# Kernel tuning notes

Measured on AMD Instinct MI355X. Metric: run time of the kernel, lower is better.

The kernel has to match this reference:

```python
import jax, jax.numpy as jnp
import numpy as np

N_FFT = 512
HOP = 256
HID = 512
VOCAB = 44
NB_BINS = 257  # n_fft//2 + 1, == max_bin
NEG = -100000.0
POS = 200000.0


def _hann(n):
    # torch.hann_window is periodic: 0.5*(1-cos(2*pi*k/N))
    return 0.5 * (1.0 - jnp.cos(2.0 * jnp.pi * jnp.arange(n, dtype=jnp.float32) / n))


def _stft_mag(x):
    # x: (B, C, T) -> (frames, B, C(mono=1), bins), magnitude spectrogram (power=1, mono mean)
    B, C, T = x.shape
    nfr = 1 + (T - N_FFT) // HOP
    idx = jnp.arange(nfr)[:, None] * HOP + jnp.arange(N_FFT)[None, :]
    frames = x.reshape(B * C, T)[:, idx] * _hann(N_FFT)      # (BC, F, n_fft)
    mag = jnp.abs(jnp.fft.rfft(frames, axis=-1))             # (BC, F, bins)
    mag = mag.reshape(B, C, nfr, N_FFT // 2 + 1).mean(axis=1, keepdims=True)
    return mag.transpose(2, 0, 1, 3)                          # (F, B, 1, bins)


def _lstm(x, wih, whh, b, reverse):
    # x: (T, B, in). torch gate order i, f, g, o. Returns hidden states (T, B, H).
    Bt, H = x.shape[1], whh.shape[1]
    def step(carry, xt):
        h, c = carry
        g = xt @ wih.T + h @ whh.T + b
        i, f, gg, o = jnp.split(g, 4, axis=-1)
        c = jax.nn.sigmoid(f) * c + jax.nn.sigmoid(i) * jnp.tanh(gg)
        h = jax.nn.sigmoid(o) * jnp.tanh(c)
        return (h, c), h
    init = (jnp.zeros((Bt, H), x.dtype), jnp.zeros((Bt, H), x.dtype))
    _, hs = jax.lax.scan(step, init, x, reverse=reverse)
    return hs


def _bilstm(x, wih, whh, b):
    # wih: (2, 4H, in) [fwd, bwd]
    hf = _lstm(x, wih[0], whh[0], b[0], False)
    hb = _lstm(x, wih[1], whh[1], b[1], True)
    return jnp.concatenate([hf, hb], axis=-1)


def _bn(x, g, b):
    # BatchNorm1d in training mode: batch statistics over axis 0, eps=1e-5
    mu = x.mean(0)
    v = ((x - mu) ** 2).mean(0)
    return g * (x - mu) * jax.lax.rsqrt(v + 1e-5) + b


def _dtw(scores):
    # dtw[n,m] = scores[n-1,m-1] + max(dtw[n-1,m], dtw[n-1,m-1]); row-wise scan
    B, N, M = scores.shape
    row0 = jnp.full((B, M + 1), NEG, scores.dtype).at[:, 0].set(POS)
    negcol = jnp.full((B, 1), NEG, scores.dtype)
    def step(prev, s):  # prev: (B, M+1), s: (B, M)
        shifted = jnp.concatenate([negcol, prev[:, :-1]], axis=1)
        new = jnp.concatenate([negcol, s + jnp.maximum(prev, shifted)[:, 1:]], axis=1)
        return new, new[:, 1:]
    _, rows = jax.lax.scan(step, row0, scores.transpose(1, 0, 2))  # (N, B, M)
    return rows.transpose(1, 0, 2)


def setup_inputs() -> dict:
    key = jax.random.key(0)
    ks = jax.random.split(key, 10)
    B, T, L = 8, 524544, 512
    s = 0.05
    H2 = HID // 2  # per-direction hidden = 256
    return {
        "x_audio": jax.random.normal(ks[0], (B, 1, T), jnp.float32),
        "text_idx": jax.random.randint(ks[1], (B, L), 0, VOCAB),
        "txt_wih": jax.random.normal(ks[2], (2, 4 * H2, VOCAB), jnp.float32) * s,
        "txt_whh": jax.random.normal(ks[3], (2, 4 * H2, H2), jnp.float32) * s,
        "txt_b": jax.random.normal(ks[4], (2, 4 * H2), jnp.float32) * s,
        "w_s": jax.random.normal(ks[5], (HID, HID), jnp.float32) / np.sqrt(HID).astype(np.float32),
        "fc1_w": jax.random.normal(ks[6], (HID, NB_BINS), jnp.float32) * s,
        "bn1_g": jnp.ones((HID,), jnp.float32),
        "bn1_b": jnp.zeros((HID,), jnp.float32),
        "input_mean": jnp.zeros((NB_BINS,), jnp.float32),
        "input_scale": jnp.ones((NB_BINS,), jnp.float32),
        "ae_wih": jax.random.normal(ks[7], (2, 2, 4 * H2, HID), jnp.float32) * s,
        "ae_whh": jax.random.normal(ks[8], (2, 2, 4 * H2, H2), jnp.float32) * s,
        "ae_b": jax.random.normal(ks[9], (2, 2, 4 * H2), jnp.float32) * s,
    }


def reference(x_audio, text_idx, txt_wih, txt_whh, txt_b, w_s, fc1_w, bn1_g, bn1_b,
              input_mean, input_scale, ae_wih, ae_whh, ae_b):
    mag = _stft_mag(x_audio)                 # (F, B, 1, bins)
    nfr, B, C, _ = mag.shape
    # text encoder (batch_first LSTM -> time-major internally)
    oneh = jax.nn.one_hot(text_idx, VOCAB, dtype=mag.dtype)           # (B, L, V)
    h = _bilstm(oneh.transpose(1, 0, 2), txt_wih, txt_whh, txt_b)     # (L, B, HID)
    h = h.transpose(1, 0, 2)                                          # (B, L, HID)
    # audio front-end
    x = (mag[..., :NB_BINS] + input_mean) * input_scale
    x = x.reshape(nfr * B, C * NB_BINS) @ fc1_w.T
    x = jnp.tanh(_bn(x, bn1_g, bn1_b)).reshape(nfr, B, HID)
    # 2-layer bidirectional audio encoder LSTM (dropout inactive / eval)
    for l in range(2):
        x = _bilstm(x, ae_wih[l], ae_whh[l], ae_b[l])
    x = x.transpose(1, 0, 2)                                          # (B, F, HID)
    side = jnp.einsum('hk,blk->bhl', w_s, h)                          # (B, HID, L)
    scores = jnp.einsum('bfh,bhl->bfl', x, side)                      # (B, F, L)
    return _dtw(scores)
```

## Files before the change

kernel.cpp:

```cpp
#include <hip/hip_runtime.h>
#include <hip/hip_bf16.h>

#define NFR    2048
#define BATCHN 8
#define NFFT   512
#define HOPSZ  256
#define BINS   257
#define HIDDEN 512
#define LTXT   512
#define TAUD   524544
#define NEGV  -100000.0f
#define POSV   200000.0f

using short8 = __attribute__((ext_vector_type(8))) short;
using u16x8  = __attribute__((ext_vector_type(8))) unsigned short;
using f32x4  = __attribute__((ext_vector_type(4))) float;
using int4v  = __attribute__((ext_vector_type(4))) int;

__device__ __forceinline__ unsigned short f2bf(float x) {
  union { float f; unsigned u; } v; v.f = x;
  unsigned u = v.u;
  u += 0x7fffu + ((u >> 16) & 1u);
  return (unsigned short)(u >> 16);
}
__device__ __forceinline__ float bf2f(unsigned short h) {
  union { unsigned u; float f; } v; v.u = ((unsigned)h) << 16;
  return v.f;
}

__device__ __forceinline__ float fsigm(float x) {
  return __builtin_amdgcn_rcpf(1.f + __expf(-x));
}
__device__ __forceinline__ float ftanh(float x) {
  return 2.f * __builtin_amdgcn_rcpf(1.f + __expf(-2.f * x)) - 1.f;
}

__device__ __forceinline__ size_t gin2_index(int t, int dir, int b, int gt, int u) {
  int w = u >> 4, col = u & 15;
  int bh = b >> 2, rp = (b >> 1) & 1, rr = b & 1;
  return (((size_t)t * 2 + dir) * 16 + w) * 512 +
         (size_t)((((bh * 16 + col) * 2 + rp) * 4 + gt) * 2 + rr);
}

__global__ __launch_bounds__(256) void zero_kernel(int* p, int n) {
  int i = blockIdx.x * 256 + threadIdx.x;
  if (i < n) p[i] = 0;
}

__global__ __launch_bounds__(256) void stft_kernel(const float* __restrict__ x,
    const float* __restrict__ imean, const float* __restrict__ iscale,
    float* __restrict__ y)
{
  __shared__ float tab[512];
  __shared__ float xs[512];
  int f = blockIdx.x, b = blockIdx.y, tid = threadIdx.x;
  for (int m = tid; m < 512; m += 256)
    tab[m] = cosf(6.283185307179586e0f / 512.0f * (float)m);
  __syncthreads();
  const float* xb = x + (size_t)b * TAUD + (size_t)f * HOPSZ;
  for (int n = tid; n < 512; n += 256)
    xs[n] = xb[n] * 0.5f * (1.0f - tab[n]);
  __syncthreads();
  for (int k = tid; k < 257; k += 256) {
    float ar = 0.f, ai = 0.f;
    int m = 0;
    for (int n = 0; n < 512; ++n) {
      float xv = xs[n];
      ar += xv * tab[m];
      ai += xv * tab[(m + 384) & 511];
      m = (m + k) & 511;
    }
    float mag = sqrtf(ar * ar + ai * ai);
    y[((size_t)f * BATCHN + b) * BINS + k] = (mag + imean[k]) * iscale[k];
  }
}

__global__ __launch_bounds__(256) void transpose_kernel(const float* __restrict__ in,
    float* __restrict__ out, int R, int C, long inBatch, long outBatch)
{
  __shared__ float tile[32][33];
  const float* ib = in + (size_t)blockIdx.z * inBatch;
  float* ob = out + (size_t)blockIdx.z * outBatch;
  int r0 = blockIdx.y * 32, c0 = blockIdx.x * 32;
  int tx = threadIdx.x & 31, ty = threadIdx.x >> 5;
  for (int i = ty; i < 32; i += 8) {
    int r = r0 + i, c = c0 + tx;
    if (r < R && c < C) tile[i][tx] = ib[(size_t)r * C + c];
  }
  __syncthreads();
  for (int i = ty; i < 32; i += 8) {
    int c = c0 + i, r = r0 + tx;
    if (r < R && c < C) ob[(size_t)c * R + r] = tile[tx][i];
  }
}

__device__ __forceinline__ void storeval(float* p, float v) { *p = v; }
__device__ __forceinline__ void storeval(unsigned short* p, float v) { *p = f2bf(v); }

template <typename OutT>
__global__ __launch_bounds__(256) void gemm_kernel(
    const float* __restrict__ A, long lda, long strideA,
    const float* __restrict__ B, long ldb, long strideB,
    OutT* __restrict__ C, long ldc, long strideC,
    int K, const float* __restrict__ bias,
    const float* __restrict__ trA, const float* __restrict__ trB, int ginmode)
{
  __shared__ float As[16][512];
  int bz = blockIdx.z;
  A += (size_t)bz * strideA; B += (size_t)bz * strideB; C += (size_t)bz * strideC;
  int rowb = blockIdx.x * 16;
  int colb = blockIdx.y * 512;
  int tid = threadIdx.x;
  for (int r = 0; r < 16; ++r)
    for (int k = tid; k < K; k += 256) {
      float v = A[(size_t)(rowb + r) * lda + k];
      if (trA) v = tanhf(trA[k] * v + trB[k]);
      As[r][k] = v;
    }
  __syncthreads();
  float acc0[16], acc1[16];
#pragma unroll
  for (int r = 0; r < 16; ++r) { acc0[r] = 0.f; acc1[r] = 0.f; }
  int c0 = colb + tid, c1 = colb + tid + 256;
  for (int k = 0; k < K; ++k) {
    float b0 = B[(size_t)k * ldb + c0];
    float b1 = B[(size_t)k * ldb + c1];
#pragma unroll
    for (int r = 0; r < 16; ++r) {
      acc0[r] = fmaf(As[r][k], b0, acc0[r]);
      acc1[r] = fmaf(As[r][k], b1, acc1[r]);
    }
  }
  float bs0 = bias ? bias[c0] : 0.f;
  float bs1 = bias ? bias[c1] : 0.f;
  if (ginmode) {
    unsigned short* Cg = (unsigned short*)C;
    for (int r = 0; r < 16; ++r) {
      int row = rowb + r; int t = row >> 3; int b = row & 7;
      { int dir = c0 >> 10, j = c0 & 1023;
        Cg[gin2_index(t, dir, b, j >> 8, j & 255)] = f2bf(acc0[r] + bs0); }
      { int dir = c1 >> 10, j = c1 & 1023;
        Cg[gin2_index(t, dir, b, j >> 8, j & 255)] = f2bf(acc1[r] + bs1); }
    }
  } else {
    for (int r = 0; r < 16; ++r) {
      storeval(C + (size_t)(rowb + r) * ldc + c0, acc0[r] + bs0);
      storeval(C + (size_t)(rowb + r) * ldc + c1, acc1[r] + bs1);
    }
  }
}

__global__ __launch_bounds__(256) void bn_stats_kernel(const float* __restrict__ z,
                                                       float* __restrict__ stats)
{
  int rowb = blockIdx.x * 64;
  int c = threadIdx.x * 2;
  float s0 = 0, s1 = 0, q0 = 0, q1 = 0;
  for (int r = 0; r < 64; ++r) {
    const float* p = z + (size_t)(rowb + r) * 512 + c;
    float v0 = p[0], v1 = p[1];
    s0 += v0; s1 += v1; q0 += v0 * v0; q1 += v1 * v1;
  }
  atomicAdd(&stats[c], s0);       atomicAdd(&stats[c + 1], s1);
  atomicAdd(&stats[512 + c], q0); atomicAdd(&stats[512 + c + 1], q1);
}

__global__ void bn_fin_kernel(float* stats, const float* __restrict__ g,
                              const float* __restrict__ b)
{
  int h = threadIdx.x;
  float mu  = stats[h] * (1.0f / 16384.0f);
  float var = stats[512 + h] * (1.0f / 16384.0f) - mu * mu;
  float a = g[h] * rsqrtf(var + 1e-5f);
  stats[1024 + h] = a;
  stats[1536 + h] = b[h] - mu * a;
}

__global__ __launch_bounds__(256) void text_gin_kernel(const int* __restrict__ idx,
    const float* __restrict__ twT, const float* __restrict__ tb,
    unsigned short* __restrict__ gin2t)
{
  size_t i = (size_t)blockIdx.x * 256 + threadIdx.x;
  if (i >= (size_t)LTXT * 8 * 2048) return;
  int j   = i & 1023;
  int dir = (i >> 10) & 1;
  int b   = (i >> 11) & 7;
  int l   = (int)(i >> 14);
  int v = idx[b * 512 + l];
  float val = twT[((size_t)dir * 44 + v) * 1024 + j] + tb[dir * 1024 + j];
  gin2t[gin2_index(l, dir, b, j >> 8, j & 255)] = f2bf(val);
}

__global__ __launch_bounds__(1024) void lstm_kernel(
    const unsigned short* __restrict__ gA, const float* __restrict__ whA,
    float* __restrict__ outA, long ostTA, long ostBA, int TA,
    const unsigned short* __restrict__ gB, const float* __restrict__ whB,
    float* __restrict__ outB, long ostTB, long ostBB, int TB)
{
  __shared__ unsigned char hlds[2][16][256];
  int job = blockIdx.x >> 1, dir = blockIdx.x & 1;
  const unsigned short* gin2 = job ? gB : gA;
  const float* whh = job ? whB : whA;
  float* out = job ? outB : outA;
  long ostT = job ? ostTB : ostTA;
  long ostB = job ? ostBB : ostBA;
  int T = job ? TB : TA;

  int tid = threadIdx.x;
  int w = tid >> 6;
  int lane = tid & 63;
  int col = lane & 15, lg = lane >> 4;

  int4v fb[4][4];
  {
    const float* wb = whh + (size_t)dir * 1024 * 256;
#pragma unroll
    for (int gt = 0; gt < 4; ++gt) {
      const float* wr = wb + (size_t)(gt * 256 + w * 16 + col) * 256 + lg * 16;
#pragma unroll
      for (int cc = 0; cc < 4; ++cc) {
        const float* p = wr + cc * 64;
        int4v v;
#pragma unroll
        for (int e = 0; e < 4; ++e) {
          unsigned wd = 0;
#pragma unroll
          for (int by = 0; by < 4; ++by) {
            float q = rintf(p[e * 4 + by] * 256.f);
            q = fminf(fmaxf(q, -127.f), 127.f);
            wd |= ((unsigned)((int)q & 255)) << (8 * by);
          }
          v[e] = (int)wd;
        }
        fb[gt][cc] = v;
      }
    }
  }

  {
    int* hz = (int*)hlds;
    for (int i = tid; i < 2048; i += 1024) hz[i] = 0;
  }
  __syncthreads();

  float cst0 = 0.f, cst1 = 0.f;
  int b0 = 2 * lg, b1 = 2 * lg + 1;
  int u = w * 16 + col;
  int srcl = col + (lg >> 1) * 16;
  const float invS = 1.f / (256.f * 127.f);
  size_t lanebase = (size_t)(((lg >> 1) * 16 + col) * 2 + (lg & 1)) * 8;

  u16x8 gr;
  {
    int t0 = dir ? (T - 1) : 0;
    gr = *(const u16x8*)(gin2 + (((size_t)t0 * 2 + dir) * 16 + w) * 512 + lanebase);
  }

  for (int s = 0; s < T; ++s) {
    int t = dir ? (T - 1 - s) : s;
    int p = s & 1;

    int4v fa[4];
#pragma unroll
    for (int cc = 0; cc < 4; ++cc) {
      int off = col * 256 + (((cc * 64) + lg * 16) ^ ((col & 7) << 4));
      fa[cc] = *(const int4v*)((const char*)&hlds[p][0][0] + off);
    }

    int4v acc[4];
#pragma unroll
    for (int gt = 0; gt < 4; ++gt) { int4v z = {0, 0, 0, 0}; acc[gt] = z; }
#pragma unroll
    for (int cc = 0; cc < 4; ++cc) {
#pragma unroll
      for (int gt = 0; gt < 4; ++gt) {
        acc[gt] = __builtin_amdgcn_mfma_i32_16x16x64_i8(fa[cc], fb[gt][cc],
                                                        acc[gt], 0, 0, 0);
      }
    }

    float g0[4], g1[4];
#pragma unroll
    for (int gt = 0; gt < 4; ++gt) {
      int v0 = __shfl(acc[gt][0], srcl, 64);
      int v1 = __shfl(acc[gt][1], srcl, 64);
      int v2 = __shfl(acc[gt][2], srcl, 64);
      int v3 = __shfl(acc[gt][3], srcl, 64);
      int a0 = (lg & 1) ? v2 : v0;
      int a1 = (lg & 1) ? v3 : v1;
      g0[gt] = bf2f(gr[gt * 2 + 0]) + (float)a0 * invS;
      g1[gt] = bf2f(gr[gt * 2 + 1]) + (float)a1 * invS;
    }

    float gi0 = fsigm(g0[0]), gf0 = fsigm(g0[1]), gg0 = ftanh(g0[2]), go0 = fsigm(g0[3]);
    float gi1 = fsigm(g1[0]), gf1 = fsigm(g1[1]), gg1 = ftanh(g1[2]), go1 = fsigm(g1[3]);
    float c0 = gf0 * cst0 + gi0 * gg0; cst0 = c0;
    float c1 = gf1 * cst1 + gi1 * gg1; cst1 = c1;
    float h0 = go0 * ftanh(c0);
    float h1 = go1 * ftanh(c1);

    out[(size_t)t * ostT + (size_t)b0 * ostB + dir * 256 + u] = h0;
    out[(size_t)t * ostT + (size_t)b1 * ostB + dir * 256 + u] = h1;
    hlds[p ^ 1][b0][u ^ ((b0 & 7) << 4)] = (unsigned char)(int)rintf(h0 * 127.f);
    hlds[p ^ 1][b1][u ^ ((b1 & 7) << 4)] = (unsigned char)(int)rintf(h1 * 127.f);

    if (s + 1 < T) {
      int tn = dir ? (T - 2 - s) : (s + 1);
      gr = *(const u16x8*)(gin2 + (((size_t)tn * 2 + dir) * 16 + w) * 512 + lanebase);
    }
    __syncthreads();
  }
}

__global__ __launch_bounds__(256) void dtw_kernel(float* __restrict__ sc)
{
  __shared__ float P[513];
  int b = blockIdx.x, tid = threadIdx.x;
  for (int j = tid; j < 513; j += 256) P[j] = (j == 0) ? POSV : NEGV;
  __syncthreads();
  float* base = sc + (size_t)b * NFR * 512;
  for (int n = 0; n < NFR; ++n) {
    float* row = base + (size_t)n * 512;
    float s0 = row[tid], s1 = row[tid + 256];
    float v0 = s0 + fmaxf(P[tid + 1], P[tid]);
    float v1 = s1 + fmaxf(P[tid + 257], P[tid + 256]);
    __syncthreads();
    P[tid + 1] = v0; P[tid + 257] = v1;
    if (tid == 0) P[0] = NEGV;
    row[tid] = v0; row[tid + 256] = v1;
    __syncthreads();
  }
}

extern "C" void kernel_launch(void* const* d_in, const int* in_sizes, int n_in,
                              void* d_out, int out_size, void* d_ws, size_t ws_size,
                              hipStream_t stream) {
  const float* x_audio  = (const float*)d_in[0];
  const int*   text_idx = (const int*)d_in[1];
  const float* txt_wih  = (const float*)d_in[2];
  const float* txt_whh  = (const float*)d_in[3];
  const float* txt_b    = (const float*)d_in[4];
  const float* w_s      = (const float*)d_in[5];
  const float* fc1_w    = (const float*)d_in[6];
  const float* bn1_g    = (const float*)d_in[7];
  const float* bn1_b    = (const float*)d_in[8];
  const float* imean    = (const float*)d_in[9];
  const float* iscale   = (const float*)d_in[10];
  const float* ae_wih   = (const float*)d_in[11];
  const float* ae_whh   = (const float*)d_in[12];
  const float* ae_b     = (const float*)d_in[13];

  char* ws = (char*)d_ws;
  size_t off = 0;
  auto alloc = [&](size_t sz) { size_t o = off; off += (sz + 255) & ~255ull; return o; };
  size_t OFF_Y    = alloc(16384ull * 257 * 4);
  size_t OFF_WT   = alloc(257ull * 512 * 4);
  size_t OFF_TWT  = alloc(2ull * 44 * 1024 * 4);
  size_t OFF_WIHT = alloc(512ull * 2048 * 4);
  size_t OFF_Z    = alloc(16384ull * 512 * 4);
  size_t OFF_L1   = alloc(16384ull * 512 * 4);
  size_t OFF_L2   = alloc(16384ull * 512 * 4);
  size_t OFF_TXT  = alloc(8ull * 512 * 512 * 4);
  size_t OFF_GIN  = alloc(16384ull * 2048 * 2);
  size_t OFF_HTT  = OFF_GIN;
  size_t OFF_SIDE = OFF_GIN + 8ull * 512 * 512 * 4;
  size_t OFF_STATS = alloc(2048ull * 4);
  (void)ws_size; (void)in_sizes; (void)n_in; (void)out_size;

  float* y       = (float*)(ws + OFF_Y);
  float* wT      = (float*)(ws + OFF_WT);
  float* twT     = (float*)(ws + OFF_TWT);
  float* wihT    = (float*)(ws + OFF_WIHT);
  float* z       = (float*)(ws + OFF_Z);
  float* l1out   = (float*)(ws + OFF_L1);
  float* l2out   = (float*)(ws + OFF_L2);
  float* textout = (float*)(ws + OFF_TXT);
  unsigned short* gin2a = (unsigned short*)(ws + OFF_GIN);
  unsigned short* gin2t = (unsigned short*)(ws + OFF_L2);
  float* htT     = (float*)(ws + OFF_HTT);
  float* side    = (float*)(ws + OFF_SIDE);
  float* stats   = (float*)(ws + OFF_STATS);
  float* outp = (float*)d_out;

  zero_kernel<<<8, 256, 0, stream>>>((int*)(ws + OFF_STATS), 2048);

  stft_kernel<<<dim3(NFR, BATCHN), 256, 0, stream>>>(x_audio, imean, iscale, y);

  transpose_kernel<<<dim3(9, 16, 1), 256, 0, stream>>>(fc1_w, wT, 512, 257, 0, 0);
  transpose_kernel<<<dim3(2, 32, 2), 256, 0, stream>>>(txt_wih, twT, 1024, 44,
                                                       1024 * 44, 44 * 1024);

  gemm_kernel<float><<<dim3(1024, 1, 1), 256, 0, stream>>>(
      y, 257, 0, wT, 512, 0, z, 512, 0, 257, nullptr, nullptr, nullptr, 0);
  bn_stats_kernel<<<256, 256, 0, stream>>>(z, stats);
  bn_fin_kernel<<<1, 512, 0, stream>>>(stats, bn1_g, bn1_b);

  text_gin_kernel<<<32768, 256, 0, stream>>>(text_idx, twT, txt_b, gin2t);

  transpose_kernel<<<dim3(16, 64, 1), 256, 0, stream>>>(ae_wih, wihT, 2048, 512, 0, 0);
  gemm_kernel<unsigned short><<<dim3(1024, 4, 1), 256, 0, stream>>>(
      z, 512, 0, wihT, 2048, 0, gin2a, 0, 0, 512, ae_b,
      stats + 1024, stats + 1536, 1);

  lstm_kernel<<<4, 1024, 0, stream>>>(
      gin2a, ae_whh, l1out, 4096, 512, NFR,
      gin2t, txt_whh, textout, 512, 512 * 512, LTXT);

  transpose_kernel<<<dim3(16, 64, 1), 256, 0, stream>>>(
      ae_wih + 2ull * 1024 * 512, wihT, 2048, 512, 0, 0);
  gemm_kernel<unsigned short><<<dim3(1024, 4, 1), 256, 0, stream>>>(
      l1out, 512, 0, wihT, 2048, 0, gin2a, 0, 0, 512, ae_b + 2048,
      nullptr, nullptr, 1);

  lstm_kernel<<<2, 1024, 0, stream>>>(
      gin2a, ae_whh + 2ull * 1024 * 256, l2out, 4096, 512, NFR,
      gin2a, ae_whh + 2ull * 1024 * 256, l2out, 4096, 512, NFR);

  transpose_kernel<<<dim3(16, 16, 8), 256, 0, stream>>>(textout, htT, 512, 512,
                                                        512 * 512, 512 * 512);
  gemm_kernel<float><<<dim3(32, 1, 8), 256, 0, stream>>>(
      w_s, 512, 0, htT, 512, 512 * 512, side, 512, 512 * 512, 512,
      nullptr, nullptr, nullptr, 0);

  gemm_kernel<float><<<dim3(128, 1, 8), 256, 0, stream>>>(
      l2out, 4096, 512, side, 512, 512 * 512, outp, 512, (long)NFR * 512, 512,
      nullptr, nullptr, nullptr, 0);
  dtw_kernel<<<8, 256, 0, stream>>>(outp);
}
```

Measured before the change: 9.545 ms.

## Prefetch gates two steps ahead, redistribute LSTM gates via LDS, tweak STFT and DTW

The LSTM recurrence now loads gate inputs two timesteps ahead using a double register buffer. Gate accumulators are redistributed through a shared-memory buffer instead of cross-lane shuffles, which needs a new gin3 gate layout written by the GEMM and text kernels. The STFT computes the Nyquist bin with a block reduction instead of a second loop pass, and the DTW kernel prefetches the next score row before the barrier. These changes target latency on the serial LSTM and DTW chains, at the cost of more shared memory and registers in the LSTM kernel.

```diff
diff --git a/kernel.cpp b/kernel.cpp
--- a/kernel.cpp
+++ b/kernel.cpp
@@ -35,11 +35,9 @@
   return 2.f * __builtin_amdgcn_rcpf(1.f + __expf(-2.f * x)) - 1.f;
 }
 
-__device__ __forceinline__ size_t gin2_index(int t, int dir, int b, int gt, int u) {
-  int w = u >> 4, col = u & 15;
-  int bh = b >> 2, rp = (b >> 1) & 1, rr = b & 1;
-  return (((size_t)t * 2 + dir) * 16 + w) * 512 +
-         (size_t)((((bh * 16 + col) * 2 + rp) * 4 + gt) * 2 + rr);
+__device__ __forceinline__ size_t gin3_index(int t, int dir, int b, int gt, int u) {
+  return (((size_t)t * 2 + dir) * 16 + (u >> 4)) * 512 +
+         (size_t)((u & 15) * 32 + b * 4 + gt);
 }
 
 __global__ __launch_bounds__(256) void zero_kernel(int* p, int n) {
@@ -53,6 +51,7 @@
 {
   __shared__ float tab[512];
   __shared__ float xs[512];
+  __shared__ float red[4];
   int f = blockIdx.x, b = blockIdx.y, tid = threadIdx.x;
   for (int m = tid; m < 512; m += 256)
     tab[m] = cosf(6.283185307179586e0f / 512.0f * (float)m);
@@ -61,7 +60,8 @@
   for (int n = tid; n < 512; n += 256)
     xs[n] = xb[n] * 0.5f * (1.0f - tab[n]);
   __syncthreads();
-  for (int k = tid; k < 257; k += 256) {
+  {
+    int k = tid;
     float ar = 0.f, ai = 0.f;
     int m = 0;
     for (int n = 0; n < 512; ++n) {
@@ -72,6 +72,18 @@
     }
     float mag = sqrtf(ar * ar + ai * ai);
     y[((size_t)f * BATCHN + b) * BINS + k] = (mag + imean[k]) * iscale[k];
+  }
+  {
+    float part = xs[2 * tid] - xs[2 * tid + 1];
+#pragma unroll
+    for (int o = 32; o; o >>= 1) part += __shfl_down(part, o, 64);
+    if ((tid & 63) == 0) red[tid >> 6] = part;
+    __syncthreads();
+    if (tid == 0) {
+      float s = red[0] + red[1] + red[2] + red[3];
+      y[((size_t)f * BATCHN + b) * BINS + 256] =
+          (fabsf(s) + imean[256]) * iscale[256];
+    }
   }
 }
 
@@ -138,9 +150,9 @@
     for (int r = 0; r < 16; ++r) {
       int row = rowb + r; int t = row >> 3; int b = row & 7;
       { int dir = c0 >> 10, j = c0 & 1023;
-        Cg[gin2_index(t, dir, b, j >> 8, j & 255)] = f2bf(acc0[r] + bs0); }
+        Cg[gin3_index(t, dir, b, j >> 8, j & 255)] = f2bf(acc0[r] + bs0); }
       { int dir = c1 >> 10, j = c1 & 1023;
-        Cg[gin2_index(t, dir, b, j >> 8, j & 255)] = f2bf(acc1[r] + bs1); }
+        Cg[gin3_index(t, dir, b, j >> 8, j & 255)] = f2bf(acc1[r] + bs1); }
     }
   } else {
     for (int r = 0; r < 16; ++r) {
@@ -178,7 +190,7 @@
 
 __global__ __launch_bounds__(256) void text_gin_kernel(const int* __restrict__ idx,
     const float* __restrict__ twT, const float* __restrict__ tb,
-    unsigned short* __restrict__ gin2t)
+    unsigned short* __restrict__ gin3t)
 {
   size_t i = (size_t)blockIdx.x * 256 + threadIdx.x;
   if (i >= (size_t)LTXT * 8 * 2048) return;
@@ -188,7 +200,7 @@
   int l   = (int)(i >> 14);
   int v = idx[b * 512 + l];
   float val = twT[((size_t)dir * 44 + v) * 1024 + j] + tb[dir * 1024 + j];
-  gin2t[gin2_index(l, dir, b, j >> 8, j & 255)] = f2bf(val);
+  gin3t[gin3_index(l, dir, b, j >> 8, j & 255)] = f2bf(val);
 }
 
 __global__ __launch_bounds__(1024) void lstm_kernel(
@@ -198,8 +210,9 @@
     float* __restrict__ outB, long ostTB, long ostBB, int TB)
 {
   __shared__ unsigned char hlds[2][16][256];
+  __shared__ int redis[16][4][33][4];
   int job = blockIdx.x >> 1, dir = blockIdx.x & 1;
-  const unsigned short* gin2 = job ? gB : gA;
+  const unsigned short* gin3 = job ? gB : gA;
   const float* whh = job ? whB : whA;
   float* out = job ? outB : outA;
   long ostT = job ? ostTB : ostTA;
@@ -246,17 +259,22 @@
   float cst0 = 0.f, cst1 = 0.f;
   int b0 = 2 * lg, b1 = 2 * lg + 1;
   int u = w * 16 + col;
-  int srcl = col + (lg >> 1) * 16;
   const float invS = 1.f / (256.f * 127.f);
-  size_t lanebase = (size_t)(((lg >> 1) * 16 + col) * 2 + (lg & 1)) * 8;
-
-  u16x8 gr;
+  int r0i = (2 * lg) & 3;
+  int l32r = col + (lg >> 1) * 16;
+
+  const unsigned short* glane = gin3 + (size_t)dir * 8192 + (size_t)w * 512 +
+                                (size_t)(col * 32 + lg * 8);
+
+  u16x8 grA, grB;
   {
     int t0 = dir ? (T - 1) : 0;
-    gr = *(const u16x8*)(gin2 + (((size_t)t0 * 2 + dir) * 16 + w) * 512 + lanebase);
-  }
-
-  for (int s = 0; s < T; ++s) {
+    int t1 = dir ? (T - 2) : 1;
+    grA = *(const u16x8*)(glane + (size_t)t0 * 16384);
+    grB = *(const u16x8*)(glane + (size_t)t1 * 16384);
+  }
+
+  auto step = [&](int s, u16x8& gr) {
     int t = dir ? (T - 1 - s) : s;
     int p = s & 1;
 
@@ -279,17 +297,22 @@
       }
     }
 
+    if (lg < 2) {
+#pragma unroll
+      for (int r = 0; r < 4; ++r) {
+        int4v tv; tv[0] = acc[0][r]; tv[1] = acc[1][r];
+        tv[2] = acc[2][r]; tv[3] = acc[3][r];
+        *(int4v*)&redis[w][r][col + lg * 16][0] = tv;
+      }
+    }
+    int4v ga = *(const int4v*)&redis[w][r0i][l32r][0];
+    int4v gb = *(const int4v*)&redis[w][r0i + 1][l32r][0];
+
     float g0[4], g1[4];
 #pragma unroll
     for (int gt = 0; gt < 4; ++gt) {
-      int v0 = __shfl(acc[gt][0], srcl, 64);
-      int v1 = __shfl(acc[gt][1], srcl, 64);
-      int v2 = __shfl(acc[gt][2], srcl, 64);
-      int v3 = __shfl(acc[gt][3], srcl, 64);
-      int a0 = (lg & 1) ? v2 : v0;
-      int a1 = (lg & 1) ? v3 : v1;
-      g0[gt] = bf2f(gr[gt * 2 + 0]) + (float)a0 * invS;
-      g1[gt] = bf2f(gr[gt * 2 + 1]) + (float)a1 * invS;
+      g0[gt] = bf2f(gr[gt])     + (float)ga[gt] * invS;
+      g1[gt] = bf2f(gr[4 + gt]) + (float)gb[gt] * invS;
     }
 
     float gi0 = fsigm(g0[0]), gf0 = fsigm(g0[1]), gg0 = ftanh(g0[2]), go0 = fsigm(g0[3]);
@@ -304,11 +327,16 @@
     hlds[p ^ 1][b0][u ^ ((b0 & 7) << 4)] = (unsigned char)(int)rintf(h0 * 127.f);
     hlds[p ^ 1][b1][u ^ ((b1 & 7) << 4)] = (unsigned char)(int)rintf(h1 * 127.f);
 
-    if (s + 1 < T) {
-      int tn = dir ? (T - 2 - s) : (s + 1);
-      gr = *(const u16x8*)(gin2 + (((size_t)tn * 2 + dir) * 16 + w) * 512 + lanebase);
+    if (s + 2 < T) {
+      int tn = dir ? (T - 3 - s) : (s + 2);
+      gr = *(const u16x8*)(glane + (size_t)tn * 16384);
     }
     __syncthreads();
+  };
+
+  for (int s = 0; s < T; s += 2) {
+    step(s, grA);
+    step(s + 1, grB);
   }
 }
 
@@ -319,11 +347,13 @@
   for (int j = tid; j < 513; j += 256) P[j] = (j == 0) ? POSV : NEGV;
   __syncthreads();
   float* base = sc + (size_t)b * NFR * 512;
+  float s0 = base[tid], s1 = base[tid + 256];
   for (int n = 0; n < NFR; ++n) {
     float* row = base + (size_t)n * 512;
-    float s0 = row[tid], s1 = row[tid + 256];
-    float v0 = s0 + fmaxf(P[tid + 1], P[tid]);
-    float v1 = s1 + fmaxf(P[tid + 257], P[tid + 256]);
+    float t0 = s0, t1 = s1;
+    if (n + 1 < NFR) { s0 = row[512 + tid]; s1 = row[768 + tid]; }
+    float v0 = t0 + fmaxf(P[tid + 1], P[tid]);
+    float v1 = t1 + fmaxf(P[tid + 257], P[tid + 256]);
     __syncthreads();
     P[tid + 1] = v0; P[tid + 257] = v1;
     if (tid == 0) P[0] = NEGV;
@@ -375,8 +405,8 @@
   float* l1out   = (float*)(ws + OFF_L1);
   float* l2out   = (float*)(ws + OFF_L2);
   float* textout = (float*)(ws + OFF_TXT);
-  unsigned short* gin2a = (unsigned short*)(ws + OFF_GIN);
-  unsigned short* gin2t = (unsigned short*)(ws + OFF_L2);
+  unsigned short* gin3a = (unsigned short*)(ws + OFF_GIN);
+  unsigned short* gin3t = (unsigned short*)(ws + OFF_L2);
   float* htT     = (float*)(ws + OFF_HTT);
   float* side    = (float*)(ws + OFF_SIDE);
   float* stats   = (float*)(ws + OFF_STATS);
@@ -395,26 +425,26 @@
   bn_stats_kernel<<<256, 256, 0, stream>>>(z, stats);
   bn_fin_kernel<<<1, 512, 0, stream>>>(stats, bn1_g, bn1_b);
 
-  text_gin_kernel<<<32768, 256, 0, stream>>>(text_idx, twT, txt_b, gin2t);
+  text_gin_kernel<<<32768, 256, 0, stream>>>(text_idx, twT, txt_b, gin3t);
 
   transpose_kernel<<<dim3(16, 64, 1), 256, 0, stream>>>(ae_wih, wihT, 2048, 512, 0, 0);
   gemm_kernel<unsigned short><<<dim3(1024, 4, 1), 256, 0, stream>>>(
-      z, 512, 0, wihT, 2048, 0, gin2a, 0, 0, 512, ae_b,
+      z, 512, 0, wihT, 2048, 0, gin3a, 0, 0, 512, ae_b,
       stats + 1024, stats + 1536, 1);
 
   lstm_kernel<<<4, 1024, 0, stream>>>(
-      gin2a, ae_whh, l1out, 4096, 512, NFR,
-      gin2t, txt_whh, textout, 512, 512 * 512, LTXT);
+      gin3a, ae_whh, l1out, 4096, 512, NFR,
+      gin3t, txt_whh, textout, 512, 512 * 512, LTXT);
 
   transpose_kernel<<<dim3(16, 64, 1), 256, 0, stream>>>(
       ae_wih + 2ull * 1024 * 512, wihT, 2048, 512, 0, 0);
   gemm_kernel<unsigned short><<<dim3(1024, 4, 1), 256, 0, stream>>>(
-      l1out, 512, 0, wihT, 2048, 0, gin2a, 0, 0, 512, ae_b + 2048,
+      l1out, 512, 0, wihT, 2048, 0, gin3a, 0, 0, 512, ae_b + 2048,
       nullptr, nullptr, 1);
 
   lstm_kernel<<<2, 1024, 0, stream>>>(
-      gin2a, ae_whh + 2ull * 1024 * 256, l2out, 4096, 512, NFR,
-      gin2a, ae_whh + 2ull * 1024 * 256, l2out, 4096, 512, NFR);
+      gin3a, ae_whh + 2ull * 1024 * 256, l2out, 4096, 512, NFR,
+      gin3a, ae_whh + 2ull * 1024 * 256, l2out, 4096, 512, NFR);
 
   transpose_kernel<<<dim3(16, 16, 8), 256, 0, stream>>>(textout, htT, 512, 512,
                                                         512 * 512, 512 * 512);
```

Measured after the change: 9.203 ms. -3.6%, faster.
